# Optimization experiments

Hardware: AMD Instinct MI355X
Metric: run time of the kernel (lower is better)

Reference implementation:

```python
import jax, jax.numpy as jnp
import numpy as np

# Dimensions
N = 12288      # fact nodes (batched graph)
B = 64         # examples in batch
R = 36         # image regions per example (hardcoded .repeat(36,1) in source)
E = 196608     # fact-graph edges (avg degree 16)
D_IN = 512     # in_dims
D_OUT = 512    # out_dims
P = 256        # img_att_proj_dim
D_IMG = 1024   # img_dim


def setup_inputs() -> dict:
    key = jax.random.key(0)
    ks = jax.random.split(key, 12)

    def w(k, shape, fan_in):
        return jax.random.normal(k, shape, dtype=jnp.float32) / np.float32(np.sqrt(fan_in))

    return {
        "h": jax.random.normal(ks[0], (N, D_IN), dtype=jnp.float32),
        "img_feats": jax.random.normal(ks[1], (B, R, D_IMG), dtype=jnp.float32),
        "batch_ids": jax.random.randint(ks[2], (N,), 0, B, dtype=jnp.int32),
        "src": jax.random.randint(ks[3], (E,), 0, N, dtype=jnp.int32),
        "dst": jax.random.randint(ks[4], (E,), 0, N, dtype=jnp.int32),
        # cross_att_fact_proj
        "Wf": w(ks[5], (D_IN, P), D_IN), "bf": jnp.zeros((P,), jnp.float32),
        # cross_att_img_proj
        "Wi": w(ks[6], (D_IMG, P), D_IMG), "bi": jnp.zeros((P,), jnp.float32),
        # att_proj (P -> 1)
        "Wa": w(ks[7], (P, 1), P), "ba": jnp.zeros((1,), jnp.float32),
        # node_fc
        "Wn": w(ks[8], (D_IN, D_OUT), D_IN), "bn": jnp.zeros((D_OUT,), jnp.float32),
        # img_fc
        "Wim": w(ks[9], (D_IMG, D_OUT), D_IMG), "bim": jnp.zeros((D_OUT,), jnp.float32),
        # apply_fc (2*out -> out)
        "Wap": w(ks[10], (2 * D_OUT, D_OUT), 2 * D_OUT), "bap": jnp.zeros((D_OUT,), jnp.float32),
    }


def reference(h, img_feats, batch_ids, src, dst,
              Wf, bf, Wi, bi, Wa, ba, Wn, bn, Wim, bim, Wap, bap):
    # ---- apply_node: cross-modal attention over the node's 36 image regions ----
    node_proj = h @ Wf + bf                                   # [N, P]
    img_proj = img_feats @ Wi + bi                            # [B, R, P]
    img_proj_n = img_proj[batch_ids]                          # [N, R, P] gather per node's example
    logits = (jnp.tanh(node_proj[:, None, :] + img_proj_n) @ Wa)[..., 0] + ba[0]  # [N, R]
    att = jax.nn.softmax(logits, axis=1)                      # softmax over 36 regions
    img_n = img_feats[batch_ids]                              # [N, R, D_IMG]
    img = jnp.einsum("nr,nrd->nd", att, img_n)               # [N, D_IMG] attended image feature
    h1 = h @ Wn + bn                                          # node_fc updates 'h' [N, D_OUT]

    # ---- update_all: copy_src('h') messages, sum reduce over in-neighbors ----
    neigh = jax.ops.segment_sum(h1[src], dst, num_segments=N)  # [N, D_OUT]
    msg = neigh + img @ Wim + bim                              # [N, D_OUT]

    # ---- reduce: concat + apply_fc + relu ----
    out = jax.nn.relu(jnp.concatenate([msg, h1], axis=1) @ Wap + bap)  # [N, D_OUT]
    return out
```

## Files before the change

### kernel.cpp

```cpp
#include <hip/hip_runtime.h>
#include <cstdint>
#include <cstddef>

#define N_NODES 12288
#define B_EX    64
#define R_REG   36
#define E_EDGES 196608
#define DD_IN   512
#define DD_OUT  512
#define P_DIM   256
#define D_IMG   1024
#define TANH_C  2.885390081777927f
#define MAXD    128

#define A2_LD     1024
#define NEIGH_OFF 0
#define H1_OFF    512

typedef unsigned short ushort;
typedef __bf16 bf16x8 __attribute__((ext_vector_type(8)));
typedef float f32x4 __attribute__((ext_vector_type(4)));
typedef ushort ushort4v __attribute__((ext_vector_type(4)));
typedef ushort ushort8v __attribute__((ext_vector_type(8)));

__device__ __forceinline__ ushort f2bf(float f) {
    uint32_t u = __float_as_uint(f);
    uint32_t r = (u + 0x7fffu + ((u >> 16) & 1u)) >> 16;
    return (ushort)r;
}
__device__ __forceinline__ float bf2f(ushort u) {
    return __uint_as_float(((uint32_t)u) << 16);
}
__device__ __forceinline__ void gload_lds16(const void* g, void* l) {
    __builtin_amdgcn_global_load_lds((const __attribute__((address_space(1))) void*)g,
                                     (__attribute__((address_space(3))) void*)l, 16, 0, 0);
}
__device__ __forceinline__ void stage_f32(const float* __restrict__ src, void* ldsDst) {
    float4 v0 = *(const float4*)src;
    float4 v1 = *(const float4*)(src + 4);
    ushort8v o;
    o[0] = f2bf(v0.x); o[1] = f2bf(v0.y); o[2] = f2bf(v0.z); o[3] = f2bf(v0.w);
    o[4] = f2bf(v1.x); o[5] = f2bf(v1.y); o[6] = f2bf(v1.z); o[7] = f2bf(v1.w);
    *(ushort8v*)ldsDst = o;
}
__device__ __forceinline__ float fexp2(float x) {
    float r; asm("v_exp_f32 %0, %1" : "=v"(r) : "v"(x)); return r;
}
__device__ __forceinline__ float frcp(float x) {
    float r; asm("v_rcp_f32 %0, %1" : "=v"(r) : "v"(x)); return r;
}
__device__ __forceinline__ float exp2c(float x) {
    return fexp2(fminf(fmaxf(x, -30.f), 30.f));
}
__device__ __forceinline__ int xcd_swz(int lin, int nwg) {
    if ((nwg & 7) == 0) return (lin & 7) * (nwg >> 3) + (lin >> 3);
    return lin;
}

#define PCVT_BLKS (N_NODES * DD_IN / 4 / 256)
#define TR_BLKS   352
#define ZERO_INTS N_NODES
#define ZERO_BLKS (ZERO_INTS / 256)
__global__ __launch_bounds__(256) void preamble(
    const float* __restrict__ h, ushort* __restrict__ h_bf,
    const float* __restrict__ Wf, const float* __restrict__ Wn,
    const float* __restrict__ Wi, const float* __restrict__ Wap,
    ushort* __restrict__ WfnT, ushort* __restrict__ WiZT,
    ushort* __restrict__ Wap1T, ushort* __restrict__ BT2,
    int* __restrict__ zero_p)
{
    if (blockIdx.x < PCVT_BLKS) {
        int i = blockIdx.x * 256 + threadIdx.x;
        float4 v = ((const float4*)h)[i];
        ushort4v o;
        o[0] = f2bf(v.x); o[1] = f2bf(v.y); o[2] = f2bf(v.z); o[3] = f2bf(v.w);
        ((ushort4v*)h_bf)[i] = o;
        return;
    }
    if (blockIdx.x >= PCVT_BLKS + TR_BLKS) {
        int i = (blockIdx.x - PCVT_BLKS - TR_BLKS) * 256 + threadIdx.x;
        if (i < ZERO_INTS) zero_p[i] = 0;
        return;
    }
    int t = blockIdx.x - PCVT_BLKS;
    const float* W; ushort* WT; int N, ldt, gx;
    if (t < 32)       { W = Wf;  WT = WfnT;                        N = 256; ldt = 512;  gx = 4; }
    else if (t < 96)  { W = Wn;  WT = WfnT + 256 * 512;            N = 512; ldt = 512;  gx = 8; t -= 32; }
    else if (t < 160) { W = Wi;  WT = WiZT;                        N = 256; ldt = 1024; gx = 4; t -= 96; }
    else if (t < 224) { W = Wap; WT = Wap1T;                       N = 512; ldt = 512;  gx = 8; t -= 160; }
    else if (t < 288) { W = Wap; WT = BT2 + NEIGH_OFF;             N = 512; ldt = 1024; gx = 8; t -= 224; }
    else              { W = Wap + 512 * 512; WT = BT2 + H1_OFF;    N = 512; ldt = 1024; gx = 8; t -= 288; }
    const int n0 = (t % gx) * 64, k0 = (t / gx) * 64;

    __shared__ float tt[64][65];
    const int tx = threadIdx.x & 15, ty = threadIdx.x >> 4;
#pragma unroll
    for (int r = 0; r < 4; ++r) {
        float4 v = *(const float4*)&W[(size_t)(k0 + ty * 4 + r) * N + n0 + tx * 4];
        tt[ty * 4 + r][tx * 4 + 0] = v.x;
        tt[ty * 4 + r][tx * 4 + 1] = v.y;
        tt[ty * 4 + r][tx * 4 + 2] = v.z;
        tt[ty * 4 + r][tx * 4 + 3] = v.w;
    }
    __syncthreads();
    const int nl = threadIdx.x >> 2, kq = (threadIdx.x & 3) * 16;
    ushort u[16] __attribute__((aligned(16)));
#pragma unroll
    for (int c = 0; c < 16; ++c) u[c] = f2bf(tt[kq + c][nl]);
    ushort* d = &WT[(size_t)(n0 + nl) * ldt + k0 + kq];
    *(ushort8v*)d = *(ushort8v*)&u[0];
    *(ushort8v*)(d + 8) = *(ushort8v*)&u[8];
}

#define ECNT_BLKS (E_EDGES / 256)
__global__ __launch_bounds__(256) void k2_scatter_sort_wp(
    const int* __restrict__ src, const int* __restrict__ dst,
    const int* __restrict__ bid,
    int* __restrict__ cur, int* __restrict__ ssrc2, int* __restrict__ nlist,
    const ushort* __restrict__ Wap1T, const float* __restrict__ Wim,
    ushort* __restrict__ WiZT)
{
    __shared__ ushort As[128 * 64];
    __shared__ ushort Bs[128 * 64];
    if (blockIdx.x < ECNT_BLKS) {
        int i = blockIdx.x * 256 + threadIdx.x;
        int d = dst[i];
        int p = atomicAdd(&cur[d], 1);
        if (p < MAXD) ssrc2[(size_t)d * MAXD + p] = src[i];
        return;
    }
    if (blockIdx.x == ECNT_BLKS) {
        __shared__ int bc[B_EX];
        __shared__ int bo[B_EX];
        if (threadIdx.x < B_EX) bc[threadIdx.x] = 0;
        __syncthreads();
        for (int i = threadIdx.x; i < N_NODES; i += 256)
            atomicAdd(&bc[bid[i]], 1);
        __syncthreads();
        if (threadIdx.x == 0) {
            int acc = 0;
            for (int i = 0; i < B_EX; ++i) { bo[i] = acc; acc += bc[i]; }
        }
        __syncthreads();
        if (threadIdx.x < B_EX) bc[threadIdx.x] = 0;
        __syncthreads();
        for (int i = threadIdx.x; i < N_NODES; i += 256) {
            int b = bid[i];
            int p = bo[b] + atomicAdd(&bc[b], 1);
            nlist[p] = i;
        }
        return;
    }
    const int K = DD_IN;
    const int tid = threadIdx.x;
    const int lane = tid & 63;
    const int wid = tid >> 6;
    const int wm = wid >> 1, wn = wid & 1;
    const int lin = blockIdx.x - (ECNT_BLKS + 1);
    const int m0 = (lin >> 3) * 128, n0 = (lin & 7) * 128;

    f32x4 acc[4][4] = {};
    const int srow = tid >> 3;
    const int schk = tid & 7;
    const char* AsB = (const char*)As;
    const char* BsB = (const char*)Bs;

    for (int k0 = 0; k0 < K; k0 += 64) {
#pragma unroll
        for (int i = 0; i < 4; ++i) {
            int row = i * 32 + srow;
            int ca = (schk ^ (row & 7)) * 8;
            gload_lds16(Wap1T + (size_t)(m0 + row) * K + k0 + ca,
                        (char*)As + i * 4096 + wid * 1024);
            stage_f32(Wim + (size_t)(n0 + row) * K + k0 + ca,
                      (char*)Bs + i * 4096 + wid * 1024 + lane * 16);
        }
        __syncthreads();
#pragma unroll
        for (int kk = 0; kk < 2; ++kk) {
            const int kc = kk * 4 + (lane >> 4);
            bf16x8 af[4], bfr[4];
#pragma unroll
            for (int i = 0; i < 4; ++i) {
                int row = wm * 64 + i * 16 + (lane & 15);
                af[i] = *(const bf16x8*)(AsB + row * 128 + ((kc ^ (row & 7)) << 4));
            }
#pragma unroll
            for (int j = 0; j < 4; ++j) {
                int col = wn * 64 + j * 16 + (lane & 15);
                bfr[j] = *(const bf16x8*)(BsB + col * 128 + ((kc ^ (col & 7)) << 4));
            }
#pragma unroll
            for (int i = 0; i < 4; ++i)
#pragma unroll
                for (int j = 0; j < 4; ++j)
                    acc[i][j] = __builtin_amdgcn_mfma_f32_16x16x32_bf16(af[i], bfr[j], acc[i][j], 0, 0, 0);
        }
        __syncthreads();
    }

#pragma unroll
    for (int i = 0; i < 4; ++i)
#pragma unroll
        for (int j = 0; j < 4; ++j)
#pragma unroll
            for (int q = 0; q < 4; ++q) {
                int row = m0 + wm * 64 + i * 16 + (lane >> 4) * 4 + q;
                int col = n0 + wn * 64 + j * 16 + (lane & 15);
                WiZT[(size_t)(256 + row) * D_IMG + col] = f2bf(acc[i][j][q]);
            }
}

#define IMGZ_BASE 2
#define FF_BASE   110
__global__ __launch_bounds__(256) void k3_imgz_ff(
    const float* __restrict__ bim, const float* __restrict__ Wap,
    const float* __restrict__ bap, float* __restrict__ bp,
    const float* __restrict__ imgf, const ushort* __restrict__ WiZT,
    const float* __restrict__ bi, ushort* __restrict__ img_projb,
    ushort* __restrict__ Z,
    const ushort* __restrict__ h_bf, const ushort* __restrict__ WfnT,
    const float* __restrict__ biasF, const float* __restrict__ biasN,
    float* __restrict__ node_proj_s, ushort* __restrict__ A2)
{
    __shared__ ushort As[128 * 64];
    __shared__ ushort Bs[128 * 64];
    const int t = threadIdx.x;
    if (blockIdx.x < IMGZ_BASE) {
        int n = blockIdx.x * 256 + t;
        float s = bap[n];
        for (int k = 0; k < DD_OUT; ++k) s += bim[k] * Wap[(size_t)k * DD_OUT + n];
        bp[n] = s;
        return;
    }
    const int lane = t & 63;
    const int wid = t >> 6;
    if (blockIdx.x < FF_BASE) {
        const int K = D_IMG;
        const int wm = wid >> 1, wn = wid & 1;
        const int lin = blockIdx.x - IMGZ_BASE;
        const int m0 = (lin / 6) * 128, n0 = (lin % 6) * 128;

        f32x4 acc[4][4] = {};
        const int srow = t >> 3;
        const int schk = t & 7;
        const char* AsB = (const char*)As;
        const char* BsB = (const char*)Bs;

        for (int k0 = 0; k0 < K; k0 += 64) {
#pragma unroll
            for (int i = 0; i < 4; ++i) {
                int row = i * 32 + srow;
                int ca = (schk ^ (row & 7)) * 8;
                stage_f32(imgf + (size_t)(m0 + row) * K + k0 + ca,
                          (char*)As + i * 4096 + wid * 1024 + lane * 16);
                gload_lds16(WiZT + (size_t)(n0 + row) * K + k0 + ca,
                            (char*)Bs + i * 4096 + wid * 1024);
            }
            __syncthreads();
#pragma unroll
            for (int kk = 0; kk < 2; ++kk) {
                const int kc = kk * 4 + (lane >> 4);
                bf16x8 af[4], bfr[4];
#pragma unroll
                for (int i = 0; i < 4; ++i) {
                    int row = wm * 64 + i * 16 + (lane & 15);
                    af[i] = *(const bf16x8*)(AsB + row * 128 + ((kc ^ (row & 7)) << 4));
                }
#pragma unroll
                for (int j = 0; j < 4; ++j) {
                    int col = wn * 64 + j * 16 + (lane & 15);
                    bfr[j] = *(const bf16x8*)(BsB + col * 128 + ((kc ^ (col & 7)) << 4));
                }
#pragma unroll
                for (int i = 0; i < 4; ++i)
#pragma unroll
                    for (int j = 0; j < 4; ++j)
                        acc[i][j] = __builtin_amdgcn_mfma_f32_16x16x32_bf16(af[i], bfr[j], acc[i][j], 0, 0, 0);
            }
            __syncthreads();
        }

        if (n0 < 256) {
#pragma unroll
            for (int i = 0; i < 4; ++i)
#pragma unroll
                for (int j = 0; j < 4; ++j)
#pragma unroll
                    for (int q = 0; q < 4; ++q) {
                        int row = m0 + wm * 64 + i * 16 + (lane >> 4) * 4 + q;
                        int col = n0 + wn * 64 + j * 16 + (lane & 15);
                        img_projb[(size_t)row * P_DIM + col] =
                            f2bf(exp2c((acc[i][j][q] + bi[col]) * TANH_C));
                    }
        } else {
#pragma unroll
            for (int i = 0; i < 4; ++i)
#pragma unroll
                for (int j = 0; j < 4; ++j)
#pragma unroll
                    for (int q = 0; q < 4; ++q) {
                        int row = m0 + wm * 64 + i * 16 + (lane >> 4) * 4 + q;
                        int col = n0 - 256 + wn * 64 + j * 16 + (lane & 15);
                        Z[(size_t)row * DD_OUT + col] = f2bf(acc[i][j][q]);
                    }
        }
        return;
    }
    const int K = DD_IN;
    const int lin = xcd_swz(blockIdx.x - FF_BASE, 1152);
    const int m0 = (lin / 12) * 128, n0 = (lin % 12) * 64;

    f32x4 acc[2][4] = {};
    const int srow = t >> 3;
    const int schk = t & 7;
    const char* AsB = (const char*)As;
    const char* BsB = (const char*)Bs;

    for (int k0 = 0; k0 < K; k0 += 64) {
#pragma unroll
        for (int i = 0; i < 4; ++i) {
            int row = i * 32 + srow;
            int ca = (schk ^ (row & 7)) * 8;
            gload_lds16(h_bf + (size_t)(m0 + row) * K + k0 + ca,
                        (char*)As + i * 4096 + wid * 1024);
        }
#pragma unroll
        for (int i = 0; i < 2; ++i) {
            int row = i * 32 + srow;
            int cb = (schk ^ (row & 7)) * 8;
            gload_lds16(WfnT + (size_t)(n0 + row) * K + k0 + cb,
                        (char*)Bs + i * 4096 + wid * 1024);
        }
        __syncthreads();
#pragma unroll
        for (int kk = 0; kk < 2; ++kk) {
            const int kc = kk * 4 + (lane >> 4);
            bf16x8 af[2], bfr[4];
#pragma unroll
            for (int i = 0; i < 2; ++i) {
                int row = wid * 32 + i * 16 + (lane & 15);
                af[i] = *(const bf16x8*)(AsB + row * 128 + ((kc ^ (row & 7)) << 4));
            }
#pragma unroll
            for (int j = 0; j < 4; ++j) {
                int col = j * 16 + (lane & 15);
                bfr[j] = *(const bf16x8*)(BsB + col * 128 + ((kc ^ (col & 7)) << 4));
            }
#pragma unroll
            for (int i = 0; i < 2; ++i)
#pragma unroll
                for (int j = 0; j < 4; ++j)
                    acc[i][j] = __builtin_amdgcn_mfma_f32_16x16x32_bf16(af[i], bfr[j], acc[i][j], 0, 0, 0);
        }
        __syncthreads();
    }

    if (n0 < 256) {
#pragma unroll
        for (int i = 0; i < 2; ++i)
#pragma unroll
            for (int j = 0; j < 4; ++j)
#pragma unroll
                for (int q = 0; q < 4; ++q) {
                    int row = m0 + wid * 32 + i * 16 + (lane >> 4) * 4 + q;
                    int col = n0 + j * 16 + (lane & 15);
                    node_proj_s[(size_t)row * P_DIM + col] =
                        exp2c((acc[i][j][q] + biasF[col]) * TANH_C);
                }
    } else {
#pragma unroll
        for (int i = 0; i < 2; ++i)
#pragma unroll
            for (int j = 0; j < 4; ++j)
#pragma unroll
                for (int q = 0; q < 4; ++q) {
                    int row = m0 + wid * 32 + i * 16 + (lane >> 4) * 4 + q;
                    int col = n0 - 256 + j * 16 + (lane & 15);
                    A2[(size_t)row * A2_LD + H1_OFF + col] = f2bf(acc[i][j][q] + biasN[col]);
                }
    }
}

__global__ __launch_bounds__(256) void k4_att(
    const float* __restrict__ Enp, const ushort* __restrict__ Eip,
    const int* __restrict__ batch_ids, const float* __restrict__ Wa,
    const ushort* __restrict__ Z, ushort* __restrict__ imgz,
    const int* __restrict__ nlist)
{
    __shared__ float red[4][R_REG][20];
    const int lane = threadIdx.x & 63;
    const int wv = threadIdx.x >> 6;
    const int n = nlist[blockIdx.x * 4 + wv];
    const int b = batch_ids[n];

    const float4 en = *(const float4*)(Enp + (size_t)n * P_DIM + 4 * lane);
    const float4 wa = *(const float4*)(Wa + 4 * lane);
    const ushort* ip0 = Eip + (size_t)b * R_REG * P_DIM + 4 * lane;

#pragma unroll
    for (int r = 0; r < R_REG; ++r) {
        ushort4v ip = *(const ushort4v*)(ip0 + (size_t)r * P_DIM);
        float u0 = fmaf(en.x, bf2f(ip[0]), 1.f);
        float u1 = fmaf(en.y, bf2f(ip[1]), 1.f);
        float u2 = fmaf(en.z, bf2f(ip[2]), 1.f);
        float u3 = fmaf(en.w, bf2f(ip[3]), 1.f);
        float p01 = u0 * u1, p23 = u2 * u3;
        float n01 = fmaf(wa.x, u1, wa.y * u0);
        float n23 = fmaf(wa.z, u3, wa.w * u2);
        float N = fmaf(n01, p23, n23 * p01);
        float p = N * frcp(p01 * p23);
        p += __shfl_xor(p, 16);
        p += __shfl_xor(p, 32);
        if (lane < 16) red[wv][r][lane] = p;
    }
    __syncthreads();

    float logit = -INFINITY;
    if (lane < R_REG) {
        const float* row = &red[wv][lane][0];
        float4 a = *(const float4*)row;
        float4 bq = *(const float4*)(row + 4);
        float4 c = *(const float4*)(row + 8);
        float4 d = *(const float4*)(row + 12);
        float s01 = ((a.x + a.y) + (a.z + a.w)) + ((bq.x + bq.y) + (bq.z + bq.w));
        float s23 = ((c.x + c.y) + (c.z + c.w)) + ((d.x + d.y) + (d.z + d.w));
        logit = -2.f * (s01 + s23);
    }
    float m = logit;
#pragma unroll
    for (int o = 32; o; o >>= 1) m = fmaxf(m, __shfl_xor(m, o));
    float e = (lane < R_REG) ? __expf(logit - m) : 0.f;
    float s = e;
#pragma unroll
    for (int o = 32; o; o >>= 1) s += __shfl_xor(s, o);
    float inv_s = frcp(s);
    if (lane < R_REG) red[wv][lane][16] = e * inv_s;

    float az[8] = {};
    const ushort* zb = Z + (size_t)b * R_REG * DD_OUT + lane * 8;
#pragma unroll 4
    for (int r = 0; r < R_REG; ++r) {
        uint4 zv = *(const uint4*)(zb + (size_t)r * DD_OUT);
        float a = red[wv][r][16];
        az[0] = fmaf(a, bf2f((ushort)(zv.x & 0xffffu)), az[0]);
        az[1] = fmaf(a, bf2f((ushort)(zv.x >> 16)),     az[1]);
        az[2] = fmaf(a, bf2f((ushort)(zv.y & 0xffffu)), az[2]);
        az[3] = fmaf(a, bf2f((ushort)(zv.y >> 16)),     az[3]);
        az[4] = fmaf(a, bf2f((ushort)(zv.z & 0xffffu)), az[4]);
        az[5] = fmaf(a, bf2f((ushort)(zv.z >> 16)),     az[5]);
        az[6] = fmaf(a, bf2f((ushort)(zv.w & 0xffffu)), az[6]);
        az[7] = fmaf(a, bf2f((ushort)(zv.w >> 16)),     az[7]);
    }
    ushort8v zo;
#pragma unroll
    for (int i = 0; i < 8; ++i) zo[i] = f2bf(az[i]);
    *(ushort8v*)(imgz + (size_t)n * DD_OUT + lane * 8) = zo;
}

__device__ __forceinline__ void acc8(float* a, uint4 v) {
    a[0] += bf2f((ushort)(v.x & 0xffffu)); a[1] += bf2f((ushort)(v.x >> 16));
    a[2] += bf2f((ushort)(v.y & 0xffffu)); a[3] += bf2f((ushort)(v.y >> 16));
    a[4] += bf2f((ushort)(v.z & 0xffffu)); a[5] += bf2f((ushort)(v.z >> 16));
    a[6] += bf2f((ushort)(v.w & 0xffffu)); a[7] += bf2f((ushort)(v.w >> 16));
}

__global__ __launch_bounds__(256) void k5_gather(
    const int* __restrict__ cur, const int* __restrict__ ssrc2,
    const ushort* __restrict__ A2h1, ushort* __restrict__ A2nb)
{
    const int lane = threadIdx.x & 63;
    const int wv = threadIdx.x >> 6;
    const int n = blockIdx.x * 4 + wv;
    int dcnt = cur[n];
    if (dcnt > MAXD) dcnt = MAXD;
    const int* es = ssrc2 + (size_t)n * MAXD;

    float a[8] = {};
    int e = 0;
    for (; e + 4 <= dcnt; e += 4) {
        int s0 = es[e], s1 = es[e + 1], s2 = es[e + 2], s3 = es[e + 3];
        uint4 v0 = *(const uint4*)(A2h1 + (size_t)s0 * A2_LD + lane * 8);
        uint4 v1 = *(const uint4*)(A2h1 + (size_t)s1 * A2_LD + lane * 8);
        uint4 v2 = *(const uint4*)(A2h1 + (size_t)s2 * A2_LD + lane * 8);
        uint4 v3 = *(const uint4*)(A2h1 + (size_t)s3 * A2_LD + lane * 8);
        acc8(a, v0); acc8(a, v1); acc8(a, v2); acc8(a, v3);
    }
    for (; e < dcnt; ++e) {
        int s0 = es[e];
        uint4 v0 = *(const uint4*)(A2h1 + (size_t)s0 * A2_LD + lane * 8);
        acc8(a, v0);
    }
    ushort8v o;
#pragma unroll
    for (int i = 0; i < 8; ++i) o[i] = f2bf(a[i]);
    *(ushort8v*)(A2nb + (size_t)n * A2_LD + lane * 8) = o;
}

__global__ __launch_bounds__(256) void gemm_out(
    const ushort* __restrict__ A, const ushort* __restrict__ BT,
    const float* __restrict__ bias, const ushort* __restrict__ Cadd,
    float* __restrict__ Cf)
{
    __shared__ ushort As[128 * 64];
    __shared__ ushort Bs[64 * 64];
    const int K = A2_LD;
    const int tid = threadIdx.x;
    const int lane = tid & 63;
    const int wid = tid >> 6;
    const int lin = xcd_swz(blockIdx.y * 8 + blockIdx.x, 768);
    const int m0 = (lin >> 3) * 128, n0 = (lin & 7) * 64;

    f32x4 acc[2][4] = {};
    const int srow = tid >> 3;
    const int schk = tid & 7;
    const char* AsB = (const char*)As;
    const char* BsB = (const char*)Bs;

    for (int k0 = 0; k0 < K; k0 += 64) {
#pragma unroll
        for (int i = 0; i < 4; ++i) {
            int row = i * 32 + srow;
            int ca = (schk ^ (row & 7)) * 8;
            gload_lds16(A + (size_t)(m0 + row) * K + k0 + ca,
                        (char*)As + i * 4096 + wid * 1024);
        }
#pragma unroll
        for (int i = 0; i < 2; ++i) {
            int row = i * 32 + srow;
            int cb = (schk ^ (row & 7)) * 8;
            gload_lds16(BT + (size_t)(n0 + row) * K + k0 + cb,
                        (char*)Bs + i * 4096 + wid * 1024);
        }
        __syncthreads();
#pragma unroll
        for (int kk = 0; kk < 2; ++kk) {
            const int kc = kk * 4 + (lane >> 4);
            bf16x8 af[2], bfr[4];
#pragma unroll
            for (int i = 0; i < 2; ++i) {
                int row = wid * 32 + i * 16 + (lane & 15);
                af[i] = *(const bf16x8*)(AsB + row * 128 + ((kc ^ (row & 7)) << 4));
            }
#pragma unroll
            for (int j = 0; j < 4; ++j) {
                int col = j * 16 + (lane & 15);
                bfr[j] = *(const bf16x8*)(BsB + col * 128 + ((kc ^ (col & 7)) << 4));
            }
#pragma unroll
            for (int i = 0; i < 2; ++i)
#pragma unroll
                for (int j = 0; j < 4; ++j)
                    acc[i][j] = __builtin_amdgcn_mfma_f32_16x16x32_bf16(af[i], bfr[j], acc[i][j], 0, 0, 0);
        }
        __syncthreads();
    }

#pragma unroll
    for (int i = 0; i < 2; ++i)
#pragma unroll
        for (int j = 0; j < 4; ++j)
#pragma unroll
            for (int q = 0; q < 4; ++q) {
                int row = m0 + wid * 32 + i * 16 + (lane >> 4) * 4 + q;
                int col = n0 + j * 16 + (lane & 15);
                float v = acc[i][j][q] + bias[col] + bf2f(Cadd[(size_t)row * DD_OUT + col]);
                Cf[(size_t)row * DD_OUT + col] = fmaxf(v, 0.f);
            }
}

extern "C" void kernel_launch(void* const* d_in, const int* in_sizes, int n_in,
                              void* d_out, int out_size, void* d_ws, size_t ws_size,
                              hipStream_t stream) {
    const float* h         = (const float*)d_in[0];
    const float* img_feats = (const float*)d_in[1];
    const int*   batch_ids = (const int*)d_in[2];
    const int*   src       = (const int*)d_in[3];
    const int*   dst       = (const int*)d_in[4];
    const float* Wf  = (const float*)d_in[5];
    const float* bf  = (const float*)d_in[6];
    const float* Wi  = (const float*)d_in[7];
    const float* bi  = (const float*)d_in[8];
    const float* Wa  = (const float*)d_in[9];
    const float* Wn  = (const float*)d_in[11];
    const float* bn  = (const float*)d_in[12];
    const float* Wim = (const float*)d_in[13];
    const float* bim = (const float*)d_in[14];
    const float* Wap = (const float*)d_in[15];
    const float* bap = (const float*)d_in[16];
    float* out = (float*)d_out;
    float* ws  = (float*)d_ws;

    ushort* A2      = (ushort*)(ws + 0);
    ushort* imgz    = (ushort*)(ws + 6291456);
    float*  node_proj = ws + 9437184;
    ushort* img_projb = (ushort*)(ws + 12582912);
    ushort* Z      = (ushort*)(ws + 12877824);
    ushort* h_bf   = (ushort*)(ws + 13467648);
    ushort* WfnT   = (ushort*)(ws + 16613376);
    ushort* WiZT   = (ushort*)(ws + 16809984);
    ushort* Wap1T  = (ushort*)(ws + 17203200);
    ushort* BT2    = (ushort*)(ws + 17334272);
    float*  bprime = ws + 17596416;
    int* cur   = (int*)(ws + 17596928);
    int* nlist = cur + N_NODES;
    int* ssrc2 = nlist + N_NODES;

    dim3 blk(256);

    preamble<<<dim3(PCVT_BLKS + TR_BLKS + ZERO_BLKS), blk, 0, stream>>>(
        h, h_bf, Wf, Wn, Wi, Wap, WfnT, WiZT, Wap1T, BT2, cur);
    k2_scatter_sort_wp<<<dim3(ECNT_BLKS + 1 + 32), blk, 0, stream>>>(
        src, dst, batch_ids, cur, ssrc2, nlist, Wap1T, Wim, WiZT);
    k3_imgz_ff<<<dim3(FF_BASE + 1152), blk, 0, stream>>>(
        bim, Wap, bap, bprime,
        img_feats, WiZT, bi, img_projb, Z,
        h_bf, WfnT, bf, bn, node_proj, A2);
    k4_att<<<dim3(N_NODES / 4), blk, 0, stream>>>(
        node_proj, img_projb, batch_ids, Wa, Z, imgz, nlist);
    k5_gather<<<dim3(N_NODES / 4), blk, 0, stream>>>(
        cur, ssrc2, A2 + H1_OFF, A2 + NEIGH_OFF);
    gemm_out<<<dim3(8, 96), blk, 0, stream>>>(A2, BT2, bprime, imgz, out);
}
```

Measured before the change: 173.9 us.

## Stage per-example image projections and Z into LDS shared across 16 nodes

```diff
diff --git a/kernel.cpp b/kernel.cpp
--- a/kernel.cpp
+++ b/kernel.cpp
@@ -382,80 +382,113 @@
     }
 }
 
-__global__ __launch_bounds__(256) void k4_att(
+#define K4_NPB 16
+__global__ __launch_bounds__(512) void k4_att(
     const float* __restrict__ Enp, const ushort* __restrict__ Eip,
     const int* __restrict__ batch_ids, const float* __restrict__ Wa,
     const ushort* __restrict__ Z, ushort* __restrict__ imgz,
     const int* __restrict__ nlist)
 {
-    __shared__ float red[4][R_REG][20];
-    const int lane = threadIdx.x & 63;
-    const int wv = threadIdx.x >> 6;
-    const int n = nlist[blockIdx.x * 4 + wv];
-    const int b = batch_ids[n];
-
-    const float4 en = *(const float4*)(Enp + (size_t)n * P_DIM + 4 * lane);
+    __shared__ ushort eip_s[R_REG * P_DIM];
+    __shared__ ushort z_s[R_REG * DD_OUT];
+    __shared__ float red[8][R_REG][20];
+    const int tid = threadIdx.x;
+    const int lane = tid & 63;
+    const int wv = tid >> 6;
+    const int base = blockIdx.x * K4_NPB;
+    const int b0 = batch_ids[nlist[base]];
+
+    {
+        const ushort8v* se = (const ushort8v*)(Eip + (size_t)b0 * R_REG * P_DIM);
+        ushort8v* de = (ushort8v*)eip_s;
+        for (int i = tid; i < R_REG * P_DIM / 8; i += 512) de[i] = se[i];
+        const ushort8v* sz = (const ushort8v*)(Z + (size_t)b0 * R_REG * DD_OUT);
+        ushort8v* dz = (ushort8v*)z_s;
+        for (int i = tid; i < R_REG * DD_OUT / 8; i += 512) dz[i] = sz[i];
+    }
+    __syncthreads();
+
     const float4 wa = *(const float4*)(Wa + 4 * lane);
-    const ushort* ip0 = Eip + (size_t)b * R_REG * P_DIM + 4 * lane;
-
-#pragma unroll
-    for (int r = 0; r < R_REG; ++r) {
-        ushort4v ip = *(const ushort4v*)(ip0 + (size_t)r * P_DIM);
-        float u0 = fmaf(en.x, bf2f(ip[0]), 1.f);
-        float u1 = fmaf(en.y, bf2f(ip[1]), 1.f);
-        float u2 = fmaf(en.z, bf2f(ip[2]), 1.f);
-        float u3 = fmaf(en.w, bf2f(ip[3]), 1.f);
-        float p01 = u0 * u1, p23 = u2 * u3;
-        float n01 = fmaf(wa.x, u1, wa.y * u0);
-        float n23 = fmaf(wa.z, u3, wa.w * u2);
-        float N = fmaf(n01, p23, n23 * p01);
-        float p = N * frcp(p01 * p23);
-        p += __shfl_xor(p, 16);
-        p += __shfl_xor(p, 32);
-        if (lane < 16) red[wv][r][lane] = p;
-    }
-    __syncthreads();
-
-    float logit = -INFINITY;
-    if (lane < R_REG) {
-        const float* row = &red[wv][lane][0];
-        float4 a = *(const float4*)row;
-        float4 bq = *(const float4*)(row + 4);
-        float4 c = *(const float4*)(row + 8);
-        float4 d = *(const float4*)(row + 12);
-        float s01 = ((a.x + a.y) + (a.z + a.w)) + ((bq.x + bq.y) + (bq.z + bq.w));
-        float s23 = ((c.x + c.y) + (c.z + c.w)) + ((d.x + d.y) + (d.z + d.w));
-        logit = -2.f * (s01 + s23);
-    }
-    float m = logit;
-#pragma unroll
-    for (int o = 32; o; o >>= 1) m = fmaxf(m, __shfl_xor(m, o));
-    float e = (lane < R_REG) ? __expf(logit - m) : 0.f;
-    float s = e;
-#pragma unroll
-    for (int o = 32; o; o >>= 1) s += __shfl_xor(s, o);
-    float inv_s = frcp(s);
-    if (lane < R_REG) red[wv][lane][16] = e * inv_s;
-
-    float az[8] = {};
-    const ushort* zb = Z + (size_t)b * R_REG * DD_OUT + lane * 8;
+
+    for (int j = 0; j < 2; ++j) {
+        const int n = nlist[base + wv * 2 + j];
+        const int b = batch_ids[n];
+        const float4 en = *(const float4*)(Enp + (size_t)n * P_DIM + 4 * lane);
+        const bool inlds = (b == b0);
+
+        auto region = [&](int r, ushort4v ip) {
+            float u0 = fmaf(en.x, bf2f(ip[0]), 1.f);
+            float u1 = fmaf(en.y, bf2f(ip[1]), 1.f);
+            float u2 = fmaf(en.z, bf2f(ip[2]), 1.f);
+            float u3 = fmaf(en.w, bf2f(ip[3]), 1.f);
+            float p01 = u0 * u1, p23 = u2 * u3;
+            float n01 = fmaf(wa.x, u1, wa.y * u0);
+            float n23 = fmaf(wa.z, u3, wa.w * u2);
+            float N = fmaf(n01, p23, n23 * p01);
+            float p = N * frcp(p01 * p23);
+            p += __shfl_xor(p, 16);
+            p += __shfl_xor(p, 32);
+            if (lane < 16) red[wv][r][lane] = p;
+        };
+        if (inlds) {
+#pragma unroll
+            for (int r = 0; r < R_REG; ++r)
+                region(r, *(const ushort4v*)(eip_s + r * P_DIM + 4 * lane));
+        } else {
+            const ushort* ip0 = Eip + (size_t)b * R_REG * P_DIM + 4 * lane;
+#pragma unroll
+            for (int r = 0; r < R_REG; ++r)
+                region(r, *(const ushort4v*)(ip0 + (size_t)r * P_DIM));
+        }
+
+        float logit = -INFINITY;
+        if (lane < R_REG) {
+            const float* row = &red[wv][lane][0];
+            float4 a = *(const float4*)row;
+            float4 bq = *(const float4*)(row + 4);
+            float4 c = *(const float4*)(row + 8);
+            float4 d = *(const float4*)(row + 12);
+            float s01 = ((a.x + a.y) + (a.z + a.w)) + ((bq.x + bq.y) + (bq.z + bq.w));
+            float s23 = ((c.x + c.y) + (c.z + c.w)) + ((d.x + d.y) + (d.z + d.w));
+            logit = -2.f * (s01 + s23);
+        }
+        float m = logit;
+#pragma unroll
+        for (int o = 32; o; o >>= 1) m = fmaxf(m, __shfl_xor(m, o));
+        float e = (lane < R_REG) ? __expf(logit - m) : 0.f;
+        float s = e;
+#pragma unroll
+        for (int o = 32; o; o >>= 1) s += __shfl_xor(s, o);
+        float inv_s = frcp(s);
+        if (lane < R_REG) red[wv][lane][16] = e * inv_s;
+
+        float az[8] = {};
+        auto zstep = [&](int r, uint4 zv) {
+            float a = red[wv][r][16];
+            az[0] = fmaf(a, bf2f((ushort)(zv.x & 0xffffu)), az[0]);
+            az[1] = fmaf(a, bf2f((ushort)(zv.x >> 16)),     az[1]);
+            az[2] = fmaf(a, bf2f((ushort)(zv.y & 0xffffu)), az[2]);
+            az[3] = fmaf(a, bf2f((ushort)(zv.y >> 16)),     az[3]);
+            az[4] = fmaf(a, bf2f((ushort)(zv.z & 0xffffu)), az[4]);
+            az[5] = fmaf(a, bf2f((ushort)(zv.z >> 16)),     az[5]);
+            az[6] = fmaf(a, bf2f((ushort)(zv.w & 0xffffu)), az[6]);
+            az[7] = fmaf(a, bf2f((ushort)(zv.w >> 16)),     az[7]);
+        };
+        if (inlds) {
 #pragma unroll 4
-    for (int r = 0; r < R_REG; ++r) {
-        uint4 zv = *(const uint4*)(zb + (size_t)r * DD_OUT);
-        float a = red[wv][r][16];
-        az[0] = fmaf(a, bf2f((ushort)(zv.x & 0xffffu)), az[0]);
-        az[1] = fmaf(a, bf2f((ushort)(zv.x >> 16)),     az[1]);
-        az[2] = fmaf(a, bf2f((ushort)(zv.y & 0xffffu)), az[2]);
-        az[3] = fmaf(a, bf2f((ushort)(zv.y >> 16)),     az[3]);
-        az[4] = fmaf(a, bf2f((ushort)(zv.z & 0xffffu)), az[4]);
-        az[5] = fmaf(a, bf2f((ushort)(zv.z >> 16)),     az[5]);
-        az[6] = fmaf(a, bf2f((ushort)(zv.w & 0xffffu)), az[6]);
-        az[7] = fmaf(a, bf2f((ushort)(zv.w >> 16)),     az[7]);
-    }
-    ushort8v zo;
-#pragma unroll
-    for (int i = 0; i < 8; ++i) zo[i] = f2bf(az[i]);
-    *(ushort8v*)(imgz + (size_t)n * DD_OUT + lane * 8) = zo;
+            for (int r = 0; r < R_REG; ++r)
+                zstep(r, *(const uint4*)(z_s + r * DD_OUT + lane * 8));
+        } else {
+            const ushort* zb = Z + (size_t)b * R_REG * DD_OUT + lane * 8;
+#pragma unroll 4
+            for (int r = 0; r < R_REG; ++r)
+                zstep(r, *(const uint4*)(zb + (size_t)r * DD_OUT));
+        }
+        ushort8v zo;
+#pragma unroll
+        for (int i = 0; i < 8; ++i) zo[i] = f2bf(az[i]);
+        *(ushort8v*)(imgz + (size_t)n * DD_OUT + lane * 8) = zo;
+    }
 }
 
 __device__ __forceinline__ void acc8(float* a, uint4 v) {
@@ -616,7 +649,7 @@
         bim, Wap, bap, bprime,
         img_feats, WiZT, bi, img_projb, Z,
         h_bf, WfnT, bf, bn, node_proj, A2);
-    k4_att<<<dim3(N_NODES / 4), blk, 0, stream>>>(
+    k4_att<<<dim3(N_NODES / K4_NPB), dim3(512), 0, stream>>>(
         node_proj, img_projb, batch_ids, Wa, Z, imgz, nlist);
     k5_gather<<<dim3(N_NODES / 4), blk, 0, stream>>>(
         cur, ssrc2, A2 + H1_OFF, A2 + NEIGH_OFF);
```

Result: slower. 181.8 us (+4.5%).
